# Performance work log

Measured on AMD Instinct MI355X. Metric: run time of the kernel, lower is better.

The kernel has to match this reference:

```python
import jax, jax.numpy as jnp
import numpy as np

MAGBIAS = 0.01
INV_SQRT2 = np.float32(1.0 / np.sqrt(2.0))


def _reflect(x, minx, maxx):
    # Half-sample symmetric reflection of indices (static numpy; matches dtcwt reflect()).
    rng = maxx - minx
    mod = np.fmod(x - minx, 2.0 * rng)
    mod = np.where(mod < 0, mod + 2.0 * rng, mod)
    out = np.where(mod >= rng, 2.0 * rng - mod, mod) + minx
    return np.round(out).astype(np.int64)


def _symm_pad(l, m):
    return _reflect(np.arange(-m, l + m, dtype=np.float64), -0.5, l - 0.5)


def _depthwise(X, h, axis, stride):
    # Per-channel 1-D correlation along rows (axis=2) or cols (axis=3), NCHW, like F.conv2d(groups=ch).
    ch = X.shape[1]
    if axis == 2:
        k = h.reshape(1, 1, -1, 1)
        strides = (stride, 1)
    else:
        k = h.reshape(1, 1, 1, -1)
        strides = (1, stride)
    k = jnp.tile(k, (ch, 1, 1, 1)).astype(X.dtype)
    return jax.lax.conv_general_dilated(
        X, k, window_strides=strides, padding='VALID',
        dimension_numbers=('NCHW', 'OIHW', 'NCHW'), feature_group_count=ch)


def colfilter(X, h):
    m = h.shape[0] // 2
    xe = _symm_pad(X.shape[2], m)
    return _depthwise(X[:, :, xe, :], h, axis=2, stride=1)


def rowfilter(X, h):
    m = h.shape[0] // 2
    xe = _symm_pad(X.shape[3], m)
    return _depthwise(X[:, :, :, xe], h, axis=3, stride=1)


def coldfilt(X, ha, hb, highpass):
    # Dual-tree decimated column filtering with a quarter-shift pair; output rows = r // 2.
    b, ch, r, c = X.shape
    m = ha.shape[0]
    xe = _symm_pad(r, m)
    ya = _depthwise(X[:, :, xe[2::2], :], ha, axis=2, stride=2)  # (b,ch,r/4,c)
    yb = _depthwise(X[:, :, xe[3::2], :], hb, axis=2, stride=2)
    first, second = (yb, ya) if highpass else (ya, yb)
    return jnp.stack([first, second], axis=3).reshape(b, ch, r // 2, c)


def rowdfilt(X, ha, hb, highpass):
    b, ch, r, c = X.shape
    m = ha.shape[0]
    xe = _symm_pad(c, m)
    ya = _depthwise(X[:, :, :, xe[2::2]], ha, axis=3, stride=2)
    yb = _depthwise(X[:, :, :, xe[3::2]], hb, axis=3, stride=2)
    first, second = (yb, ya) if highpass else (ya, yb)
    return jnp.stack([first, second], axis=4).reshape(b, ch, r, c // 2)


def q2c(y):
    # Quads -> two complex subbands (real, imag): the DTCWT butterfly combine.
    y = y * INV_SQRT2
    a = y[..., 0::2, 0::2]
    b = y[..., 0::2, 1::2]
    c = y[..., 1::2, 0::2]
    d = y[..., 1::2, 1::2]
    return (a - d, b + c), (a + d, b - c)


def _stack_orients(lh, hl, hh):
    (d15r, d15i), (d165r, d165i) = q2c(lh)
    (d45r, d45i), (d135r, d135i) = q2c(hh)
    (d75r, d75i), (d105r, d105i) = q2c(hl)
    reals = jnp.stack([d15r, d45r, d75r, d105r, d135r, d165r], axis=1)
    imags = jnp.stack([d15i, d45i, d75i, d105i, d135i, d165i], axis=1)
    return reals, imags


def fwd_j1(x, h0, h1):
    # Level-1 DTCWT: undecimated separable biorthogonal filters + q2c.
    lo = rowfilter(x, h0)
    hi = rowfilter(x, h1)
    ll = colfilter(lo, h0)
    lh = colfilter(lo, h1)
    hl = colfilter(hi, h0)
    hh = colfilter(hi, h1)
    reals, imags = _stack_orients(lh, hl, hh)
    return ll, reals, imags


def fwd_j2plus(x, h0a, h1a, h0b, h1b):
    # Level-2 DTCWT: decimated quarter-shift filter pairs + q2c.
    lo = rowdfilt(x, h0b, h0a, False)
    hi = rowdfilt(x, h1b, h1a, True)
    ll = coldfilt(lo, h0b, h0a, False)
    lh = coldfilt(lo, h1b, h1a, True)
    hl = coldfilt(hi, h0b, h0a, False)
    hh = coldfilt(hi, h1b, h1a, True)
    reals, imags = _stack_orients(lh, hl, hh)
    return ll, reals, imags


def _smooth_mag(re, im, bias):
    return jnp.sqrt(re * re + im * im + bias * bias) - bias


def _avgpool2(x):
    b, ch, r, c = x.shape
    return x.reshape(b, ch, r // 2, 2, c // 2, 2).mean(axis=(3, 5))


def _scat_forward(x, h0o, h1o, h0a, h0b, h1a, h1b):
    b, ch, r, c = x.shape  # r, c multiples of 8 (input already padded)
    # First order, scale j=1
    ll, re, im = fwd_j1(x, h0o, h1o)
    s1_j1 = _smooth_mag(re, im, MAGBIAS)                      # (b,6,ch,r/2,c/2)
    # First order, scale j=2 (on the running lowpass)
    ll, re, im = fwd_j2plus(ll, h0a, h1a, h0b, h1b)           # ll: (b,ch,r/2,c/2)
    s1_j2 = _smooth_mag(re, im, MAGBIAS)                      # (b,6,ch,r/4,c/4)
    # Second order: one more octave on the first-order magnitudes
    p = s1_j1.reshape(b, 6 * ch, r // 2, c // 2)
    p, re, im = fwd_j1(p, h0o, h1o)
    s2 = _smooth_mag(re, im, MAGBIAS).reshape(b, 36, ch, r // 4, c // 4)
    s0 = _avgpool2(ll)[:, None]                               # (b,1,ch,r/4,c/4)
    s1_j1 = _avgpool2(p).reshape(b, 6, ch, r // 4, c // 4)
    Z = jnp.concatenate([s0, s1_j1, s1_j2, s2], axis=1)       # (b,49,ch,r/4,c/4)
    return Z.reshape(b, 49 * ch, r // 4, c // 4)


def setup_inputs():
    key = jax.random.key(0)
    ks = jax.random.split(key, 5)
    x = jax.random.normal(ks[0], (32, 3, 512, 512), dtype=jnp.float32)
    h0o = jax.random.normal(ks[1], (5,), dtype=jnp.float32) * 0.3
    h1o = jax.random.normal(ks[2], (7,), dtype=jnp.float32) * 0.3
    h0a = jax.random.normal(ks[3], (10,), dtype=jnp.float32) * 0.3
    h1a = jax.random.normal(ks[4], (10,), dtype=jnp.float32) * 0.3
    h0b = h0a[::-1]  # quarter-shift pair: time-reverse of the tree-a filter
    h1b = h1a[::-1]
    return {"x": x, "h0o": h0o, "h1o": h1o, "h0a": h0a, "h0b": h0b,
            "h1a": h1a, "h1b": h1b}


def reference(x, h0o, h1o, h0a, h0b, h1a, h1b):
    return _scat_forward(x, h0o, h1o, h0a, h0b, h1a, h1b)
```

## Files before the change

kernel.cpp:

```cpp
#include <hip/hip_runtime.h>

#define IS2 0.70710678118654752440f

__device__ __forceinline__ int refl(int i, int n) {
    if (i < 0) i = -1 - i;
    if (i >= n) i = 2 * n - 1 - i;
    return i;
}

__device__ __forceinline__ float smag(float re, float im) {
    return sqrtf(re * re + im * im + 1.0e-4f) - 0.01f;
}

template <int MODE, int N, int CH>
__device__ __forceinline__
void j1_tile(float* __restrict__ smem,
             const float* __restrict__ in,
             const float* __restrict__ h0,
             const float* __restrict__ h1,
             float* __restrict__ ll_out,
             float* __restrict__ mag_out,
             int img, int ty0, int tx0)
{
    const int b   = img / CH;
    const int chn = img % CH;
    const int tid = threadIdx.x;

    float* const sx  = smem;
    float* const slo = smem + 5040;
    float* const shi = sx;

    float f0[5], f1[7];
#pragma unroll
    for (int t = 0; t < 5; ++t) f0[t] = h0[t];
#pragma unroll
    for (int t = 0; t < 7; ++t) f1[t] = h1[t];

    const float* src = in + (size_t)img * N * N;

    const bool interior = (ty0 >= 3) && (ty0 + 66 <= N - 1) &&
                          (tx0 >= 4) && (tx0 + 67 <= N - 1);
    if (interior) {
        const float* bp = src + (size_t)(ty0 - 3) * N + (tx0 - 4);
        for (int e = tid; e < 70 * 18; e += 256) {
            int rr = e / 18, g = e - rr * 18;
            *(float4*)&sx[rr * 72 + 4 * g] =
                *(const float4*)(bp + (size_t)rr * N + 4 * g);
        }
    } else {
        for (int e = tid; e < 70 * 72; e += 256) {
            int rr = e / 72, cc = e - rr * 72;
            int gr = refl(ty0 - 3 + rr, N);
            int gc = refl(tx0 - 4 + cc, N);
            sx[rr * 72 + cc] = src[(size_t)gr * N + gc];
        }
    }
    __syncthreads();

    float rlo[5][4], rhi[5][4];
#pragma unroll
    for (int k = 0; k < 5; ++k) {
        int e = tid + k * 256;
        if (e < 1120) {
            int rr = e >> 4, g = e & 15;
            const float4* w4 = (const float4*)&sx[rr * 72 + 4 * g];
            float4 wa = w4[0], wb = w4[1], wc = w4[2];
            float win[12] = {wa.x, wa.y, wa.z, wa.w,
                             wb.x, wb.y, wb.z, wb.w,
                             wc.x, wc.y, wc.z, wc.w};
#pragma unroll
            for (int u = 0; u < 4; ++u) {
                float lo = 0.f, hi = 0.f;
#pragma unroll
                for (int t = 0; t < 5; ++t) lo += win[u + 2 + t] * f0[t];
#pragma unroll
                for (int t = 0; t < 7; ++t) hi += win[u + 1 + t] * f1[t];
                rlo[k][u] = lo; rhi[k][u] = hi;
            }
        }
    }
    __syncthreads();
#pragma unroll
    for (int k = 0; k < 5; ++k) {
        int e = tid + k * 256;
        if (e < 1120) {
            int rr = e >> 4, g = e & 15;
            *(float4*)&slo[rr * 64 + 4 * g] =
                make_float4(rlo[k][0], rlo[k][1], rlo[k][2], rlo[k][3]);
            *(float4*)&shi[rr * 64 + 4 * g] =
                make_float4(rhi[k][0], rhi[k][1], rhi[k][2], rhi[k][3]);
        }
    }
    __syncthreads();

    const int j     = tid & 63;
    const int rg    = tid >> 6;
    const int rbase = rg * 16;

    float clo[22], chi[22];
#pragma unroll
    for (int t = 0; t < 22; ++t) {
        clo[t] = slo[(rbase + t) * 64 + j];
        chi[t] = shi[(rbase + t) * 64 + j];
    }

    const int Nh  = N >> 1;
    const int par = j & 1;
    const int qx  = (tx0 >> 1) + (j >> 1);
    const int qy0 = (ty0 >> 1) + rg * 8;
    const int oLH = par ? 5 : 0;
    const int oHH = par ? 4 : 1;
    const int oHL = par ? 3 : 2;

    float* lcol = nullptr;
    float* pLH = nullptr; float* pHH = nullptr; float* pHL = nullptr;
    float* zLH = nullptr; float* zHH = nullptr; float* zHL = nullptr;
    float* zPL = nullptr;
    if (MODE == 0) {
        lcol = ll_out + (size_t)img * N * N + (size_t)(ty0 + rbase) * N + tx0 + j;
        const size_t planeSz = (size_t)Nh * Nh;
        const size_t qoff = (size_t)qy0 * Nh + qx;
        pLH = mag_out + ((size_t)(b * 6 + oLH) * CH + chn) * planeSz + qoff;
        pHH = mag_out + ((size_t)(b * 6 + oHH) * CH + chn) * planeSz + qoff;
        pHL = mag_out + ((size_t)(b * 6 + oHL) * CH + chn) * planeSz + qoff;
    } else {
        const int o1 = chn / 3, c3 = chn % 3;
        float* zBase = mag_out + (size_t)b * 147 * 16384 + (size_t)qy0 * 128 + qx;
        zLH = zBase + (size_t)((13 + oLH * 6 + o1) * 3 + c3) * 16384;
        zHH = zBase + (size_t)((13 + oHH * 6 + o1) * 3 + c3) * 16384;
        zHL = zBase + (size_t)((13 + oHL * 6 + o1) * 3 + c3) * 16384;
        zPL = zBase + (size_t)((1 + o1) * 3 + c3) * 16384;
    }

#pragma unroll
    for (int ii = 0; ii < 8; ++ii) {
        const int i0 = 2 * ii, i1 = 2 * ii + 1;
        float ll0 = 0.f, ll1 = 0.f, lh0 = 0.f, lh1 = 0.f;
        float hl0 = 0.f, hl1 = 0.f, hh0 = 0.f, hh1 = 0.f;
#pragma unroll
        for (int t = 0; t < 5; ++t) {
            ll0 += clo[i0 + 1 + t] * f0[t]; ll1 += clo[i1 + 1 + t] * f0[t];
            hl0 += chi[i0 + 1 + t] * f0[t]; hl1 += chi[i1 + 1 + t] * f0[t];
        }
#pragma unroll
        for (int t = 0; t < 7; ++t) {
            lh0 += clo[i0 + t] * f1[t]; lh1 += clo[i1 + t] * f1[t];
            hh0 += chi[i0 + t] * f1[t]; hh1 += chi[i1 + t] * f1[t];
        }

        float lhT = __shfl_xor(lh0, 1), lhB = __shfl_xor(lh1, 1);
        float hhT = __shfl_xor(hh0, 1), hhB = __shfl_xor(hh1, 1);
        float hlT = __shfl_xor(hl0, 1), hlB = __shfl_xor(hl1, 1);
        float mLH = smag(IS2 * (lh0 - lhB), IS2 * (lhT + lh1));
        float mHH = smag(IS2 * (hh0 - hhB), IS2 * (hhT + hh1));
        float mHL = smag(IS2 * (hl0 - hlB), IS2 * (hlT + hl1));

        if (MODE == 0) {
            lcol[(size_t)i0 * N] = ll0;
            lcol[(size_t)i1 * N] = ll1;
            pLH[ii * Nh] = mLH;
            pHH[ii * Nh] = mHH;
            pHL[ii * Nh] = mHL;
        } else {
            __builtin_nontemporal_store(mLH, zLH + ii * 128);
            __builtin_nontemporal_store(mHH, zHH + ii * 128);
            __builtin_nontemporal_store(mHL, zHL + ii * 128);
            float llT = __shfl_xor(ll0, 1), llB = __shfl_xor(ll1, 1);
            if (par == 0) {
                __builtin_nontemporal_store(
                    0.25f * (ll0 + ll1 + llT + llB), zPL + ii * 128);
            }
        }
    }
}

__device__ __forceinline__
void j2_tile(float* __restrict__ smem,
             const float* __restrict__ ll,
             const float* __restrict__ h0a, const float* __restrict__ h0b,
             const float* __restrict__ h1a, const float* __restrict__ h1b,
             float* __restrict__ Z, int img, int r0, int c0)
{
    const int b = img / 3, c = img % 3;
    const int tid = threadIdx.x;

    float* const sx   = smem;
    float* const sloP = sx;
    float* const shiP = sx + 2688;

    float fa0[10], fb0[10], fa1[10], fb1[10];
#pragma unroll
    for (int t = 0; t < 10; ++t) {
        fa0[t] = h0a[t]; fb0[t] = h0b[t];
        fa1[t] = h1a[t]; fb1[t] = h1b[t];
    }

    const float* src = ll + (size_t)img * 512 * 512;
    const int gy0 = 2 * r0 - 8, gx0 = 2 * c0 - 8;

    const bool interior = (gy0 >= 0) && (gy0 + 79 <= 511) &&
                          (gx0 >= 0) && (gx0 + 79 <= 511);
    if (interior) {
        const float* bp = src + (size_t)gy0 * 512 + gx0;
        for (int e = tid; e < 80 * 20; e += 256) {
            int rr = e / 20, g = e - rr * 20;
            *(float4*)&sx[rr * 84 + 4 * g] =
                *(const float4*)(bp + (size_t)rr * 512 + 4 * g);
        }
    } else {
        for (int e = tid; e < 80 * 80; e += 256) {
            int rr = e / 80, cc = e - rr * 80;
            int gr = refl(gy0 + rr, 512);
            int gc = refl(gx0 + cc, 512);
            sx[rr * 84 + cc] = src[(size_t)gr * 512 + gc];
        }
    }
    __syncthreads();

    const int jj  = tid & 31;
    const int odd = jj & 1;
    const int base = 2 * (jj & ~1);
    float hlo[10], hhi[10];
#pragma unroll
    for (int t = 0; t < 10; ++t) {
        hlo[t] = odd ? fa0[t] : fb0[t];
        hhi[t] = odd ? fb1[t] : fa1[t];
    }
    const int offlo = base + odd;
    const int offhi = base + 1 - odd;
    float rlo[10], rhi[10];
#pragma unroll
    for (int k = 0; k < 10; ++k) {
        int rr = (tid >> 5) + 8 * k;
        const float* row = &sx[rr * 84];
        float lo = 0.f, hi = 0.f;
#pragma unroll
        for (int t = 0; t < 10; ++t) {
            lo += row[offlo + 2 * t] * hlo[t];
            hi += row[offhi + 2 * t] * hhi[t];
        }
        rlo[k] = lo; rhi[k] = hi;
    }
    __syncthreads();
#pragma unroll
    for (int k = 0; k < 10; ++k) {
        int rr = (tid >> 5) + 8 * k;
        sloP[rr * 33 + jj] = rlo[k];
        shiP[rr * 33 + jj] = rhi[k];
    }
    __syncthreads();

    const int j = tid & 31;
    const int g = tid >> 5;

    float clo[24], chi[24];
#pragma unroll
    for (int t = 0; t < 24; ++t) {
        clo[t] = sloP[(8 * g + t) * 33 + j];
        chi[t] = shiP[(8 * g + t) * 33 + j];
    }

    const int dj  = j & 1;
    const int qx  = (c0 >> 1) + (j >> 1);
    const int qy0 = (r0 >> 1) + 2 * g;
    const int oLH = dj ? 5 : 0;
    const int oHH = dj ? 4 : 1;
    const int oHL = dj ? 3 : 2;

    float* Zb = Z + (size_t)b * 147 * 16384 + (size_t)qy0 * 128 + qx;
    float* zLH = Zb + (size_t)((7 + oLH) * 3 + c) * 16384;
    float* zHH = Zb + (size_t)((7 + oHH) * 3 + c) * 16384;
    float* zHL = Zb + (size_t)((7 + oHL) * 3 + c) * 16384;
    float* zPL = Zb + (size_t)c * 16384;

#pragma unroll
    for (int r = 0; r < 2; ++r) {
        const int off = 4 * r;
        float vll0 = 0.f, vll1 = 0.f, vlh0 = 0.f, vlh1 = 0.f;
        float vhl0 = 0.f, vhl1 = 0.f, vhh0 = 0.f, vhh1 = 0.f;
#pragma unroll
        for (int t = 0; t < 10; ++t) {
            float e0 = clo[off + 2 * t];
            float e1 = clo[off + 2 * t + 1];
            float g0 = chi[off + 2 * t];
            float g1 = chi[off + 2 * t + 1];
            vll0 += e0 * fb0[t];
            vll1 += e1 * fa0[t];
            vlh0 += e1 * fa1[t];
            vlh1 += e0 * fb1[t];
            vhl0 += g0 * fb0[t];
            vhl1 += g1 * fa0[t];
            vhh0 += g1 * fa1[t];
            vhh1 += g0 * fb1[t];
        }

        float lhT = __shfl_xor(vlh0, 1), lhB = __shfl_xor(vlh1, 1);
        float hhT = __shfl_xor(vhh0, 1), hhB = __shfl_xor(vhh1, 1);
        float hlT = __shfl_xor(vhl0, 1), hlB = __shfl_xor(vhl1, 1);
        float mLH = smag(IS2 * (vlh0 - lhB), IS2 * (lhT + vlh1));
        float mHH = smag(IS2 * (vhh0 - hhB), IS2 * (hhT + vhh1));
        float mHL = smag(IS2 * (vhl0 - hlB), IS2 * (hlT + vhl1));

        __builtin_nontemporal_store(mLH, zLH + r * 128);
        __builtin_nontemporal_store(mHH, zHH + r * 128);
        __builtin_nontemporal_store(mHL, zHL + r * 128);

        float llT = __shfl_xor(vll0, 1), llB = __shfl_xor(vll1, 1);
        if (dj == 0) {
            __builtin_nontemporal_store(
                0.25f * (vll0 + vll1 + llT + llB), zPL + r * 128);
        }
    }
}

__global__ __launch_bounds__(256, 4)
void k_j1_l1(const float* __restrict__ x,
             const float* __restrict__ h0o, const float* __restrict__ h1o,
             float* __restrict__ ll, float* __restrict__ p)
{
    __shared__ __align__(16) float smem[9520];
    j1_tile<0, 512, 3>(smem, x, h0o, h1o, ll, p,
                       blockIdx.z, blockIdx.y * 64, blockIdx.x * 64);
}

__global__ __launch_bounds__(256, 4)
void k_p23(const float* __restrict__ ll, const float* __restrict__ p,
           const float* __restrict__ h0o, const float* __restrict__ h1o,
           const float* __restrict__ h0a, const float* __restrict__ h0b,
           const float* __restrict__ h1a, const float* __restrict__ h1b,
           float* __restrict__ Z)
{
    __shared__ __align__(16) float smem[9520];
    const int B = blockIdx.x;
    if (B < 6144) {
        const int img = B >> 6, rem = B & 63;
        j2_tile(smem, ll, h0a, h0b, h1a, h1b, Z,
                img, ((rem >> 3) & 7) * 32, (rem & 7) * 32);
    } else {
        const int T = B - 6144;
        const int img = T >> 4, rem = T & 15;
        j1_tile<1, 256, 18>(smem, p, h0o, h1o, nullptr, Z,
                            img, ((rem >> 2) & 3) * 64, (rem & 3) * 64);
    }
}

extern "C" void kernel_launch(void* const* d_in, const int* in_sizes, int n_in,
                              void* d_out, int out_size, void* d_ws, size_t ws_size,
                              hipStream_t stream)
{
    const float* x   = (const float*)d_in[0];
    const float* h0o = (const float*)d_in[1];
    const float* h1o = (const float*)d_in[2];
    const float* h0a = (const float*)d_in[3];
    const float* h0b = (const float*)d_in[4];
    const float* h1a = (const float*)d_in[5];
    const float* h1b = (const float*)d_in[6];
    float* Z = (float*)d_out;

    float* ws_ll = (float*)d_ws;
    float* ws_p  = ws_ll + (size_t)32 * 3 * 512 * 512;

    dim3 blk(256);
    k_j1_l1<<<dim3(8, 8, 96), blk, 0, stream>>>(x, h0o, h1o, ws_ll, ws_p);
    k_p23<<<dim3(15360), blk, 0, stream>>>(ws_ll, ws_p, h0o, h1o,
                                           h0a, h0b, h1a, h1b, Z);
}
```

Baseline: 562.1 us.

## Interleave lo/hi filter outputs in shared memory and use packed float2 FMAs

```diff
diff --git a/kernel.cpp b/kernel.cpp
--- a/kernel.cpp
+++ b/kernel.cpp
@@ -1,4 +1,6 @@
 #include <hip/hip_runtime.h>
+
+typedef float v2f __attribute__((ext_vector_type(2)));
 
 #define IS2 0.70710678118654752440f
 
@@ -26,9 +28,8 @@
     const int chn = img % CH;
     const int tid = threadIdx.x;
 
-    float* const sx  = smem;
-    float* const slo = smem + 5040;
-    float* const shi = sx;
+    float* const sx = smem;
+    float* const s2 = smem;
 
     float f0[5], f1[7];
 #pragma unroll
@@ -57,7 +58,7 @@
     }
     __syncthreads();
 
-    float rlo[5][4], rhi[5][4];
+    float4 rA[5], rB[5];
 #pragma unroll
     for (int k = 0; k < 5; ++k) {
         int e = tid + k * 256;
@@ -68,15 +69,18 @@
             float win[12] = {wa.x, wa.y, wa.z, wa.w,
                              wb.x, wb.y, wb.z, wb.w,
                              wc.x, wc.y, wc.z, wc.w};
+            float lo[4], hi[4];
 #pragma unroll
             for (int u = 0; u < 4; ++u) {
-                float lo = 0.f, hi = 0.f;
-#pragma unroll
-                for (int t = 0; t < 5; ++t) lo += win[u + 2 + t] * f0[t];
-#pragma unroll
-                for (int t = 0; t < 7; ++t) hi += win[u + 1 + t] * f1[t];
-                rlo[k][u] = lo; rhi[k][u] = hi;
+                float l = 0.f, h = 0.f;
+#pragma unroll
+                for (int t = 0; t < 5; ++t) l += win[u + 2 + t] * f0[t];
+#pragma unroll
+                for (int t = 0; t < 7; ++t) h += win[u + 1 + t] * f1[t];
+                lo[u] = l; hi[u] = h;
             }
+            rA[k] = make_float4(lo[0], hi[0], lo[1], hi[1]);
+            rB[k] = make_float4(lo[2], hi[2], lo[3], hi[3]);
         }
     }
     __syncthreads();
@@ -85,10 +89,8 @@
         int e = tid + k * 256;
         if (e < 1120) {
             int rr = e >> 4, g = e & 15;
-            *(float4*)&slo[rr * 64 + 4 * g] =
-                make_float4(rlo[k][0], rlo[k][1], rlo[k][2], rlo[k][3]);
-            *(float4*)&shi[rr * 64 + 4 * g] =
-                make_float4(rhi[k][0], rhi[k][1], rhi[k][2], rhi[k][3]);
+            *(float4*)&s2[rr * 128 + 8 * g]     = rA[k];
+            *(float4*)&s2[rr * 128 + 8 * g + 4] = rB[k];
         }
     }
     __syncthreads();
@@ -97,12 +99,17 @@
     const int rg    = tid >> 6;
     const int rbase = rg * 16;
 
-    float clo[22], chi[22];
+    v2f w[22];
 #pragma unroll
     for (int t = 0; t < 22; ++t) {
-        clo[t] = slo[(rbase + t) * 64 + j];
-        chi[t] = shi[(rbase + t) * 64 + j];
-    }
+        w[t] = *(const v2f*)&s2[(rbase + t) * 128 + 2 * j];
+    }
+
+    v2f f0d[5], f1d[7];
+#pragma unroll
+    for (int t = 0; t < 5; ++t) f0d[t] = (v2f){f0[t], f0[t]};
+#pragma unroll
+    for (int t = 0; t < 7; ++t) f1d[t] = (v2f){f1[t], f1[t]};
 
     const int Nh  = N >> 1;
     const int par = j & 1;
@@ -135,18 +142,20 @@
 #pragma unroll
     for (int ii = 0; ii < 8; ++ii) {
         const int i0 = 2 * ii, i1 = 2 * ii + 1;
-        float ll0 = 0.f, ll1 = 0.f, lh0 = 0.f, lh1 = 0.f;
-        float hl0 = 0.f, hl1 = 0.f, hh0 = 0.f, hh1 = 0.f;
+        v2f A0 = {0.f, 0.f}, A1 = {0.f, 0.f};
+        v2f C0 = {0.f, 0.f}, C1 = {0.f, 0.f};
 #pragma unroll
         for (int t = 0; t < 5; ++t) {
-            ll0 += clo[i0 + 1 + t] * f0[t]; ll1 += clo[i1 + 1 + t] * f0[t];
-            hl0 += chi[i0 + 1 + t] * f0[t]; hl1 += chi[i1 + 1 + t] * f0[t];
+            A0 += w[i0 + 1 + t] * f0d[t];
+            A1 += w[i1 + 1 + t] * f0d[t];
         }
 #pragma unroll
         for (int t = 0; t < 7; ++t) {
-            lh0 += clo[i0 + t] * f1[t]; lh1 += clo[i1 + t] * f1[t];
-            hh0 += chi[i0 + t] * f1[t]; hh1 += chi[i1 + t] * f1[t];
-        }
+            C0 += w[i0 + t] * f1d[t];
+            C1 += w[i1 + t] * f1d[t];
+        }
+        float ll0 = A0.x, hl0 = A0.y, ll1 = A1.x, hl1 = A1.y;
+        float lh0 = C0.x, hh0 = C0.y, lh1 = C1.x, hh1 = C1.y;
 
         float lhT = __shfl_xor(lh0, 1), lhB = __shfl_xor(lh1, 1);
         float hhT = __shfl_xor(hh0, 1), hhB = __shfl_xor(hh1, 1);
@@ -184,9 +193,8 @@
     const int b = img / 3, c = img % 3;
     const int tid = threadIdx.x;
 
-    float* const sx   = smem;
-    float* const sloP = sx;
-    float* const shiP = sx + 2688;
+    float* const sx = smem;
+    float* const s2 = smem;
 
     float fa0[10], fb0[10], fa1[10], fb1[10];
 #pragma unroll
@@ -220,44 +228,38 @@
     const int jj  = tid & 31;
     const int odd = jj & 1;
     const int base = 2 * (jj & ~1);
-    float hlo[10], hhi[10];
+    v2f fp[10];
 #pragma unroll
     for (int t = 0; t < 10; ++t) {
-        hlo[t] = odd ? fa0[t] : fb0[t];
-        hhi[t] = odd ? fb1[t] : fa1[t];
-    }
-    const int offlo = base + odd;
-    const int offhi = base + 1 - odd;
-    float rlo[10], rhi[10];
+        fp[t] = odd ? (v2f){fb1[t], fa0[t]} : (v2f){fb0[t], fa1[t]};
+    }
+    v2f racc[10];
 #pragma unroll
     for (int k = 0; k < 10; ++k) {
         int rr = (tid >> 5) + 8 * k;
-        const float* row = &sx[rr * 84];
-        float lo = 0.f, hi = 0.f;
+        const float* row = &sx[rr * 84 + base];
+        v2f acc = {0.f, 0.f};
 #pragma unroll
         for (int t = 0; t < 10; ++t) {
-            lo += row[offlo + 2 * t] * hlo[t];
-            hi += row[offhi + 2 * t] * hhi[t];
-        }
-        rlo[k] = lo; rhi[k] = hi;
+            acc += (*(const v2f*)&row[2 * t]) * fp[t];
+        }
+        racc[k] = odd ? (v2f){acc.y, acc.x} : acc;
     }
     __syncthreads();
 #pragma unroll
     for (int k = 0; k < 10; ++k) {
         int rr = (tid >> 5) + 8 * k;
-        sloP[rr * 33 + jj] = rlo[k];
-        shiP[rr * 33 + jj] = rhi[k];
+        *(v2f*)&s2[rr * 64 + 2 * jj] = racc[k];
     }
     __syncthreads();
 
     const int j = tid & 31;
     const int g = tid >> 5;
 
-    float clo[24], chi[24];
+    v2f w[24];
 #pragma unroll
     for (int t = 0; t < 24; ++t) {
-        clo[t] = sloP[(8 * g + t) * 33 + j];
-        chi[t] = shiP[(8 * g + t) * 33 + j];
+        w[t] = *(const v2f*)&s2[(8 * g + t) * 64 + 2 * j];
     }
 
     const int dj  = j & 1;
@@ -280,18 +282,16 @@
         float vhl0 = 0.f, vhl1 = 0.f, vhh0 = 0.f, vhh1 = 0.f;
 #pragma unroll
         for (int t = 0; t < 10; ++t) {
-            float e0 = clo[off + 2 * t];
-            float e1 = clo[off + 2 * t + 1];
-            float g0 = chi[off + 2 * t];
-            float g1 = chi[off + 2 * t + 1];
-            vll0 += e0 * fb0[t];
-            vll1 += e1 * fa0[t];
-            vlh0 += e1 * fa1[t];
-            vlh1 += e0 * fb1[t];
-            vhl0 += g0 * fb0[t];
-            vhl1 += g1 * fa0[t];
-            vhh0 += g1 * fa1[t];
-            vhh1 += g0 * fb1[t];
+            v2f p0 = w[off + 2 * t];
+            v2f p1 = w[off + 2 * t + 1];
+            vll0 += p0.x * fb0[t];
+            vll1 += p1.x * fa0[t];
+            vlh0 += p1.x * fa1[t];
+            vlh1 += p0.x * fb1[t];
+            vhl0 += p0.y * fb0[t];
+            vhl1 += p1.y * fa0[t];
+            vhh0 += p1.y * fa1[t];
+            vhh1 += p0.y * fb1[t];
         }
 
         float lhT = __shfl_xor(vlh0, 1), lhB = __shfl_xor(vlh1, 1);
@@ -318,7 +318,7 @@
              const float* __restrict__ h0o, const float* __restrict__ h1o,
              float* __restrict__ ll, float* __restrict__ p)
 {
-    __shared__ __align__(16) float smem[9520];
+    __shared__ __align__(16) float smem[8960];
     j1_tile<0, 512, 3>(smem, x, h0o, h1o, ll, p,
                        blockIdx.z, blockIdx.y * 64, blockIdx.x * 64);
 }
@@ -330,7 +330,7 @@
            const float* __restrict__ h1a, const float* __restrict__ h1b,
            float* __restrict__ Z)
 {
-    __shared__ __align__(16) float smem[9520];
+    __shared__ __align__(16) float smem[8960];
     const int B = blockIdx.x;
     if (B < 6144) {
         const int img = B >> 6, rem = B & 63;
```

Result: no change. 559.4 us (-0.5%).
